# Kernel tuning notes

Hardware: AMD Instinct MI355X
Metric: run time of the kernel (lower is better)

Reference implementation:

```python
import jax, jax.numpy as jnp
import numpy as np

N_NODES = 100000
N_EDGES = 1600000
IN_DIM = 256
OUT_DIM = 128


def setup_inputs() -> dict:
    key = jax.random.key(0)
    k1, k2, k3, k4, k5 = jax.random.split(key, 5)
    h = jax.random.normal(k1, (N_NODES, IN_DIM), dtype=jnp.float32)
    # xavier_normal-ish scales for the two weight matrices
    W = jax.random.normal(k2, (IN_DIM, OUT_DIM), dtype=jnp.float32) * (2.0 / np.sqrt(IN_DIM + OUT_DIM))
    a = jax.random.normal(k3, (2 * OUT_DIM,), dtype=jnp.float32) * (2.0 / np.sqrt(2 * OUT_DIM + 1))
    src = jax.random.randint(k4, (N_EDGES,), 0, N_NODES, dtype=jnp.int32)
    dst = jax.random.randint(k5, (N_EDGES,), 0, N_NODES, dtype=jnp.int32)
    return {"h": h, "W": W, "a": a, "src": src, "dst": dst}


def reference(h, W, a, src, dst):
    n = h.shape[0]
    d = W.shape[1]
    z = h @ W  # [N, out_dim]
    # attn_fc([z_src || z_dst]) == z_src @ a[:d] + z_dst @ a[d:]
    el = z @ a[:d]  # [N]
    er = z @ a[d:]  # [N]
    e = jax.nn.leaky_relu(el[src] + er[dst])  # [E], torch default slope 0.01
    # per-destination (segment) softmax, numerically stable
    seg_max = jax.ops.segment_max(e, dst, num_segments=n)
    e_exp = jnp.exp(e - seg_max[dst])
    denom = jax.ops.segment_sum(e_exp, dst, num_segments=n)
    alpha = e_exp / denom[dst]  # [E]
    # weighted scatter-sum of source z into destinations
    h_out = jax.ops.segment_sum(alpha[:, None] * z[src], dst, num_segments=n)
    return h_out
```

## Files before the change

### kernel.cpp

```cpp
#include <hip/hip_runtime.h>
#include <cstdint>
#include <cstddef>

#define N_NODES 100000
#define N_EDGES 1600000
#define IN_DIM  256
#define OUT_DIM 128

#define NBUCK  196
#define BSHIFT 9
#define BNODES 512
#define BCAP   10240
#define EPB    4096

#define ENC_NEG_INF 0x00800000u
#define PAD_PAIR 0xFF7FFFFF00000000ull

typedef __attribute__((ext_vector_type(8))) short bf16x8;
typedef __attribute__((ext_vector_type(4))) float f32x4;

__device__ __forceinline__ unsigned bf16rn(float f) {
    unsigned u = __float_as_uint(f);
    return (u + 0x7FFFu + ((u >> 16) & 1u)) >> 16;
}

__global__ void init_k(int* __restrict__ bucket_cursor)
{
    int t = threadIdx.x;
    if (t < NBUCK) bucket_cursor[t] = 0;
}

__global__ void w16s_k(const float* __restrict__ W, unsigned short* __restrict__ w16s)
{
    int t = blockIdx.x * blockDim.x + threadIdx.x;
    if (t >= IN_DIM * OUT_DIM) return;
    int j  = t & 7;
    int n  = (t >> 3) & 15;
    int q  = (t >> 7) & 3;
    int c  = (t >> 9) & 7;
    int kc = t >> 12;
    int k   = kc * 32 + q * 8 + j;
    int dim = c * 16 + n;
    w16s[t] = (unsigned short)bf16rn(W[k * OUT_DIM + dim]);
}

#define LA_STRIDE 264

__global__ __launch_bounds__(256) void gemm_z_k(
    const float* __restrict__ h, const unsigned short* __restrict__ w16s,
    const float* __restrict__ a,
    unsigned short* __restrict__ z16, float* __restrict__ el, float* __restrict__ er)
{
    __shared__ unsigned short lA[64 * LA_STRIDE];
    const int t  = threadIdx.x;
    const int n0 = blockIdx.x * 64;

    #pragma unroll
    for (int p = 0; p < 16; ++p) {
        int f = p * 256 + t;
        int i = f >> 6;
        int col = (f & 63) * 4;
        float4 v = make_float4(0.f, 0.f, 0.f, 0.f);
        if (n0 + i < N_NODES)
            v = *(const float4*)&h[(size_t)(n0 + i) * IN_DIM + col];
        uint2 pk;
        pk.x = bf16rn(v.x) | (bf16rn(v.y) << 16);
        pk.y = bf16rn(v.z) | (bf16rn(v.w) << 16);
        *(uint2*)&lA[i * LA_STRIDE + col] = pk;
    }
    __syncthreads();

    const int w    = t >> 6;
    const int lane = t & 63;
    const int q    = lane >> 4;
    const int col  = lane & 15;

    f32x4 acc[8];
    #pragma unroll
    for (int c = 0; c < 8; ++c) acc[c] = (f32x4){0.f, 0.f, 0.f, 0.f};

    #pragma unroll
    for (int kc = 0; kc < 8; ++kc) {
        bf16x8 af = *(const bf16x8*)&lA[(w * 16 + col) * LA_STRIDE + kc * 32 + q * 8];
        bf16x8 bfr[8];
        #pragma unroll
        for (int c = 0; c < 8; ++c)
            bfr[c] = *(const bf16x8*)&w16s[((((kc * 8 + c) * 4 + q) * 16) + col) * 8];
        #pragma unroll
        for (int c = 0; c < 8; ++c)
            acc[c] = __builtin_amdgcn_mfma_f32_16x16x32_bf16(af, bfr[c], acc[c], 0, 0, 0);
    }

    float aL[8], aR[8];
    #pragma unroll
    for (int c = 0; c < 8; ++c) {
        aL[c] = a[c * 16 + col];
        aR[c] = a[128 + c * 16 + col];
    }
    #pragma unroll
    for (int r = 0; r < 4; ++r) {
        int node = n0 + w * 16 + q * 4 + r;
        float sl = 0.f, sr = 0.f;
        #pragma unroll
        for (int c = 0; c < 8; ++c) {
            sl += acc[c][r] * aL[c];
            sr += acc[c][r] * aR[c];
        }
        #pragma unroll
        for (int o = 1; o < 16; o <<= 1) {
            sl += __shfl_xor(sl, o, 64);
            sr += __shfl_xor(sr, o, 64);
        }
        if (node < N_NODES) {
            #pragma unroll
            for (int c = 0; c < 8; ++c)
                z16[(size_t)node * OUT_DIM + c * 16 + col] =
                    (unsigned short)bf16rn(acc[c][r]);
            if (col == 0) { el[node] = sl; er[node] = sr; }
        }
    }
}

__global__ __launch_bounds__(256) void partition_k(
    const int* __restrict__ src, const int* __restrict__ dst,
    const float* __restrict__ el, const float* __restrict__ er,
    int* __restrict__ bucket_cursor, unsigned long long* __restrict__ ebuf)
{
    __shared__ int hist[NBUCK];
    __shared__ int gbaseL[NBUCK];
    const int t = threadIdx.x;
    for (int i = t; i < NBUCK; i += 256) hist[i] = 0;
    __syncthreads();

    const int e0 = blockIdx.x * EPB;
    int bucks[16], ranks[16];
    unsigned long long pk[16];
    #pragma unroll
    for (int k = 0; k < 16; ++k) {
        int e = e0 + k * 256 + t;
        bucks[k] = -1;
        if (e < N_EDGES) {
            int s = src[e], d = dst[e];
            float v = el[s] + er[d];
            v = (v > 0.0f) ? v : 0.01f * v;
            int b = d >> BSHIFT;
            bucks[k] = b;
            ranks[k] = atomicAdd(&hist[b], 1);
            pk[k] = ((unsigned long long)__float_as_uint(v) << 32)
                  | ((unsigned)s << BSHIFT) | (unsigned)(d & (BNODES - 1));
        }
    }
    __syncthreads();
    for (int i = t; i < NBUCK; i += 256)
        gbaseL[i] = atomicAdd(&bucket_cursor[i], hist[i]);
    __syncthreads();
    #pragma unroll
    for (int k = 0; k < 16; ++k)
        if (bucks[k] >= 0)
            ebuf[(size_t)bucks[k] * BCAP + gbaseL[bucks[k]] + ranks[k]] = pk[k];
}

__global__ __launch_bounds__(256) void bucket_k(
    const int* __restrict__ bucket_cursor, const unsigned long long* __restrict__ ebuf,
    unsigned long long* __restrict__ perm, int* __restrict__ begA,
    int* __restrict__ endA, unsigned* __restrict__ emaxA)
{
    __shared__ int deg[BNODES];
    __shared__ int off[BNODES];
    __shared__ int cur[BNODES];
    __shared__ unsigned emaxL[BNODES];
    __shared__ int ssum[256];

    const int b = blockIdx.x;
    const int t = threadIdx.x;
    const int cnt = bucket_cursor[b];
    const unsigned long long* eb = ebuf + (size_t)b * BCAP;
    unsigned long long* pb = perm + (size_t)b * BCAP;

    for (int i = t; i < BNODES; i += 256) { deg[i] = 0; emaxL[i] = ENC_NEG_INF; }
    __syncthreads();

    for (int i = t; i < cnt; i += 256)
        atomicAdd(&deg[(int)(eb[i] & (BNODES - 1))], 1);
    __syncthreads();

    int d0 = deg[2 * t], d1 = deg[2 * t + 1];
    int p0 = (d0 + 3) & ~3, p1 = (d1 + 3) & ~3;
    ssum[t] = p0 + p1;
    __syncthreads();
    for (int o = 1; o < 256; o <<= 1) {
        int v = (t >= o) ? ssum[t - o] : 0;
        __syncthreads();
        ssum[t] += v;
        __syncthreads();
    }
    int excl = ssum[t] - (p0 + p1);
    off[2 * t] = excl;       cur[2 * t] = excl;
    off[2 * t + 1] = excl + p0; cur[2 * t + 1] = excl + p0;
    __syncthreads();

    for (int i = t; i < cnt; i += 256) {
        unsigned long long pv = eb[i];
        int ld = (int)(pv & (BNODES - 1));
        unsigned s  = (unsigned)((pv >> BSHIFT) & 0x1FFFFu);
        unsigned eb32 = (unsigned)(pv >> 32);
        int p = atomicAdd(&cur[ld], 1);
        pb[p] = ((unsigned long long)eb32 << 32) | s;
        unsigned enc = (eb32 & 0x80000000u) ? ~eb32 : (eb32 | 0x80000000u);
        atomicMax(&emaxL[ld], enc);
    }
    __syncthreads();

    for (int i = t; i < BNODES; i += 256) {
        int n = b * BNODES + i;
        if (n < N_NODES) {
            int d  = deg[i];
            int pd = (d + 3) & ~3;
            int o  = off[i];
            int gb = b * BCAP + o;
            begA[n]  = gb;
            endA[n]  = gb + pd;
            emaxA[n] = emaxL[i];
            for (int j = o + d; j < o + pd; ++j) pb[j] = PAD_PAIR;
        }
    }
}

__global__ __launch_bounds__(256) void node_pass_k(
    const int* __restrict__ begA, const int* __restrict__ endA,
    const unsigned* __restrict__ emaxA, const unsigned long long* __restrict__ perm,
    const unsigned* __restrict__ z16, float* __restrict__ out)
{
    int n    = (blockIdx.x * blockDim.x + threadIdx.x) >> 6;
    int lane = threadIdx.x & 63;
    if (n >= N_NODES) return;
    int beg = begA[n], end = endA[n];

    float acc0 = 0.0f, acc1 = 0.0f;
    if (end > beg) {
        unsigned u = emaxA[n];
        float mx = (u & 0x80000000u) ? __uint_as_float(u ^ 0x80000000u)
                                     : __uint_as_float(~u);
        float denom = 0.0f;
        const uint4* pp = (const uint4*)perm;
        #pragma unroll 2
        for (int i = (beg >> 2); i < (end >> 2); ++i) {
            uint4 pA = pp[2 * i];
            uint4 pB = pp[2 * i + 1];
            unsigned q0 = z16[(size_t)pA.x * 64 + lane];
            unsigned q1 = z16[(size_t)pA.z * 64 + lane];
            unsigned q2 = z16[(size_t)pB.x * 64 + lane];
            unsigned q3 = z16[(size_t)pB.z * 64 + lane];
            float w0 = __expf(__uint_as_float(pA.y) - mx);
            float w1 = __expf(__uint_as_float(pA.w) - mx);
            float w2 = __expf(__uint_as_float(pB.y) - mx);
            float w3 = __expf(__uint_as_float(pB.w) - mx);
            denom += (w0 + w1) + (w2 + w3);
            acc0 += w0 * __uint_as_float(q0 << 16)
                  + w1 * __uint_as_float(q1 << 16)
                  + w2 * __uint_as_float(q2 << 16)
                  + w3 * __uint_as_float(q3 << 16);
            acc1 += w0 * __uint_as_float(q0 & 0xFFFF0000u)
                  + w1 * __uint_as_float(q1 & 0xFFFF0000u)
                  + w2 * __uint_as_float(q2 & 0xFFFF0000u)
                  + w3 * __uint_as_float(q3 & 0xFFFF0000u);
        }
        float inv = 1.0f / denom;
        acc0 *= inv; acc1 *= inv;
    }
    *(float2*)&out[(size_t)n * OUT_DIM + lane * 2] = make_float2(acc0, acc1);
}

extern "C" void kernel_launch(void* const* d_in, const int* in_sizes, int n_in,
                              void* d_out, int out_size, void* d_ws, size_t ws_size,
                              hipStream_t stream)
{
    (void)in_sizes; (void)n_in; (void)out_size; (void)ws_size;
    const float* h = (const float*)d_in[0];
    const float* W = (const float*)d_in[1];
    const float* a = (const float*)d_in[2];
    const int* src = (const int*)d_in[3];
    const int* dst = (const int*)d_in[4];
    float* out = (float*)d_out;

    char* ws = (char*)d_ws;
    size_t off = 0;
    auto alloc = [&](size_t bytes) -> char* {
        char* p = ws + off;
        off += (bytes + 255) & ~(size_t)255;
        return p;
    };
    unsigned short* z16  = (unsigned short*)alloc((size_t)N_NODES * OUT_DIM * 2);
    unsigned short* w16s = (unsigned short*)alloc((size_t)IN_DIM * OUT_DIM * 2);
    float*    el        = (float*)   alloc((size_t)N_NODES * 4);
    float*    er        = (float*)   alloc((size_t)N_NODES * 4);
    int*      bucket_cursor = (int*) alloc((size_t)NBUCK * 4);
    unsigned long long* ebuf = (unsigned long long*)alloc((size_t)NBUCK * BCAP * 8);
    unsigned long long* perm = (unsigned long long*)alloc((size_t)NBUCK * BCAP * 8);
    int*      begA      = (int*)     alloc((size_t)N_NODES * 4);
    int*      endA      = (int*)     alloc((size_t)N_NODES * 4);
    unsigned* emaxA     = (unsigned*)alloc((size_t)N_NODES * 4);

    init_k<<<1, 256, 0, stream>>>(bucket_cursor);
    w16s_k<<<(IN_DIM * OUT_DIM + 255) / 256, 256, 0, stream>>>(W, w16s);
    gemm_z_k<<<(N_NODES + 63) / 64, 256, 0, stream>>>(h, w16s, a, z16, el, er);
    partition_k<<<(N_EDGES + EPB - 1) / EPB, 256, 0, stream>>>(src, dst, el, er,
                                                               bucket_cursor, ebuf);
    bucket_k<<<NBUCK, 256, 0, stream>>>(bucket_cursor, ebuf, perm, begA, endA, emaxA);
    node_pass_k<<<(N_NODES * 64 + 255) / 256, 256, 0, stream>>>(begA, endA, emaxA, perm,
                                                                (const unsigned*)z16, out);
}
```

Measured before the change: 309.8 us.

## Precompute softmax weights and denominators in bucket pass, halve bucket size

The bucket kernel now computes each destination's max in the counting pass, then evaluates exp(e - max) per edge, accumulates the per-node denominator in shared memory, and stores the weight instead of the raw score in the permuted edge array. The node pass then only does weighted gathers and one division, with no exp or denominator accumulation across the 64 lanes. Buckets shrink from 512 to 256 nodes, giving 391 blocks and one node per thread, which raises parallelism in the bucket kernel. The cost is an extra read of the bucket's edges, more shared-memory atomics, and a denominator summed by float atomics in nondeterministic order.

```diff
diff --git a/kernel.cpp b/kernel.cpp
--- a/kernel.cpp
+++ b/kernel.cpp
@@ -7,14 +7,13 @@
 #define IN_DIM  256
 #define OUT_DIM 128
 
-#define NBUCK  196
-#define BSHIFT 9
-#define BNODES 512
-#define BCAP   10240
+#define NBUCK  391
+#define BSHIFT 8
+#define BNODES 256
+#define BCAP   5632
 #define EPB    4096
 
 #define ENC_NEG_INF 0x00800000u
-#define PAD_PAIR 0xFF7FFFFF00000000ull
 
 typedef __attribute__((ext_vector_type(8))) short bf16x8;
 typedef __attribute__((ext_vector_type(4))) float f32x4;
@@ -26,8 +25,8 @@
 
 __global__ void init_k(int* __restrict__ bucket_cursor)
 {
-    int t = threadIdx.x;
-    if (t < NBUCK) bucket_cursor[t] = 0;
+    int i = blockIdx.x * blockDim.x + threadIdx.x;
+    if (i < NBUCK) bucket_cursor[i] = 0;
 }
 
 __global__ void w16s_k(const float* __restrict__ W, unsigned short* __restrict__ w16s)
@@ -163,12 +162,13 @@
 __global__ __launch_bounds__(256) void bucket_k(
     const int* __restrict__ bucket_cursor, const unsigned long long* __restrict__ ebuf,
     unsigned long long* __restrict__ perm, int* __restrict__ begA,
-    int* __restrict__ endA, unsigned* __restrict__ emaxA)
+    int* __restrict__ endA, float* __restrict__ denomA)
 {
     __shared__ int deg[BNODES];
     __shared__ int off[BNODES];
     __shared__ int cur[BNODES];
     __shared__ unsigned emaxL[BNODES];
+    __shared__ float denomL[BNODES];
     __shared__ int ssum[256];
 
     const int b = blockIdx.x;
@@ -177,16 +177,22 @@
     const unsigned long long* eb = ebuf + (size_t)b * BCAP;
     unsigned long long* pb = perm + (size_t)b * BCAP;
 
-    for (int i = t; i < BNODES; i += 256) { deg[i] = 0; emaxL[i] = ENC_NEG_INF; }
-    __syncthreads();
-
-    for (int i = t; i < cnt; i += 256)
-        atomicAdd(&deg[(int)(eb[i] & (BNODES - 1))], 1);
-    __syncthreads();
-
-    int d0 = deg[2 * t], d1 = deg[2 * t + 1];
-    int p0 = (d0 + 3) & ~3, p1 = (d1 + 3) & ~3;
-    ssum[t] = p0 + p1;
+    deg[t] = 0; emaxL[t] = ENC_NEG_INF; denomL[t] = 0.0f;
+    __syncthreads();
+
+    for (int i = t; i < cnt; i += 256) {
+        unsigned long long pv = eb[i];
+        int ld = (int)(pv & (BNODES - 1));
+        unsigned e32 = (unsigned)(pv >> 32);
+        unsigned enc = (e32 & 0x80000000u) ? ~e32 : (e32 | 0x80000000u);
+        atomicAdd(&deg[ld], 1);
+        atomicMax(&emaxL[ld], enc);
+    }
+    __syncthreads();
+
+    int d  = deg[t];
+    int pd = (d + 3) & ~3;
+    ssum[t] = pd;
     __syncthreads();
     for (int o = 1; o < 256; o <<= 1) {
         int v = (t >= o) ? ssum[t - o] : 0;
@@ -194,41 +200,39 @@
         ssum[t] += v;
         __syncthreads();
     }
-    int excl = ssum[t] - (p0 + p1);
-    off[2 * t] = excl;       cur[2 * t] = excl;
-    off[2 * t + 1] = excl + p0; cur[2 * t + 1] = excl + p0;
+    int excl = ssum[t] - pd;
+    off[t] = excl; cur[t] = excl;
     __syncthreads();
 
     for (int i = t; i < cnt; i += 256) {
         unsigned long long pv = eb[i];
         int ld = (int)(pv & (BNODES - 1));
-        unsigned s  = (unsigned)((pv >> BSHIFT) & 0x1FFFFu);
-        unsigned eb32 = (unsigned)(pv >> 32);
+        unsigned s = (unsigned)((pv >> BSHIFT) & 0x1FFFFu);
+        float e = __uint_as_float((unsigned)(pv >> 32));
+        unsigned u = emaxL[ld];
+        float mx = (u & 0x80000000u) ? __uint_as_float(u ^ 0x80000000u)
+                                     : __uint_as_float(~u);
+        float w = __expf(e - mx);
+        atomicAdd(&denomL[ld], w);
         int p = atomicAdd(&cur[ld], 1);
-        pb[p] = ((unsigned long long)eb32 << 32) | s;
-        unsigned enc = (eb32 & 0x80000000u) ? ~eb32 : (eb32 | 0x80000000u);
-        atomicMax(&emaxL[ld], enc);
-    }
-    __syncthreads();
-
-    for (int i = t; i < BNODES; i += 256) {
-        int n = b * BNODES + i;
-        if (n < N_NODES) {
-            int d  = deg[i];
-            int pd = (d + 3) & ~3;
-            int o  = off[i];
-            int gb = b * BCAP + o;
-            begA[n]  = gb;
-            endA[n]  = gb + pd;
-            emaxA[n] = emaxL[i];
-            for (int j = o + d; j < o + pd; ++j) pb[j] = PAD_PAIR;
-        }
+        pb[p] = ((unsigned long long)__float_as_uint(w) << 32) | s;
+    }
+    __syncthreads();
+
+    int n = b * BNODES + t;
+    if (n < N_NODES) {
+        int o  = off[t];
+        int gb = b * BCAP + o;
+        begA[n]   = gb;
+        endA[n]   = gb + pd;
+        denomA[n] = denomL[t];
+        for (int j = o + d; j < o + pd; ++j) pb[j] = 0ull;
     }
 }
 
 __global__ __launch_bounds__(256) void node_pass_k(
     const int* __restrict__ begA, const int* __restrict__ endA,
-    const unsigned* __restrict__ emaxA, const unsigned long long* __restrict__ perm,
+    const float* __restrict__ denomA, const unsigned long long* __restrict__ perm,
     const unsigned* __restrict__ z16, float* __restrict__ out)
 {
     int n    = (blockIdx.x * blockDim.x + threadIdx.x) >> 6;
@@ -238,10 +242,6 @@
 
     float acc0 = 0.0f, acc1 = 0.0f;
     if (end > beg) {
-        unsigned u = emaxA[n];
-        float mx = (u & 0x80000000u) ? __uint_as_float(u ^ 0x80000000u)
-                                     : __uint_as_float(~u);
-        float denom = 0.0f;
         const uint4* pp = (const uint4*)perm;
         #pragma unroll 2
         for (int i = (beg >> 2); i < (end >> 2); ++i) {
@@ -251,11 +251,10 @@
             unsigned q1 = z16[(size_t)pA.z * 64 + lane];
             unsigned q2 = z16[(size_t)pB.x * 64 + lane];
             unsigned q3 = z16[(size_t)pB.z * 64 + lane];
-            float w0 = __expf(__uint_as_float(pA.y) - mx);
-            float w1 = __expf(__uint_as_float(pA.w) - mx);
-            float w2 = __expf(__uint_as_float(pB.y) - mx);
-            float w3 = __expf(__uint_as_float(pB.w) - mx);
-            denom += (w0 + w1) + (w2 + w3);
+            float w0 = __uint_as_float(pA.y);
+            float w1 = __uint_as_float(pA.w);
+            float w2 = __uint_as_float(pB.y);
+            float w3 = __uint_as_float(pB.w);
             acc0 += w0 * __uint_as_float(q0 << 16)
                   + w1 * __uint_as_float(q1 << 16)
                   + w2 * __uint_as_float(q2 << 16)
@@ -265,7 +264,7 @@
                   + w2 * __uint_as_float(q2 & 0xFFFF0000u)
                   + w3 * __uint_as_float(q3 & 0xFFFF0000u);
         }
-        float inv = 1.0f / denom;
+        float inv = 1.0f / denomA[n];
         acc0 *= inv; acc1 *= inv;
     }
     *(float2*)&out[(size_t)n * OUT_DIM + lane * 2] = make_float2(acc0, acc1);
@@ -299,14 +298,14 @@
     unsigned long long* perm = (unsigned long long*)alloc((size_t)NBUCK * BCAP * 8);
     int*      begA      = (int*)     alloc((size_t)N_NODES * 4);
     int*      endA      = (int*)     alloc((size_t)N_NODES * 4);
-    unsigned* emaxA     = (unsigned*)alloc((size_t)N_NODES * 4);
-
-    init_k<<<1, 256, 0, stream>>>(bucket_cursor);
+    float*    denomA    = (float*)   alloc((size_t)N_NODES * 4);
+
+    init_k<<<(NBUCK + 255) / 256, 256, 0, stream>>>(bucket_cursor);
     w16s_k<<<(IN_DIM * OUT_DIM + 255) / 256, 256, 0, stream>>>(W, w16s);
     gemm_z_k<<<(N_NODES + 63) / 64, 256, 0, stream>>>(h, w16s, a, z16, el, er);
     partition_k<<<(N_EDGES + EPB - 1) / EPB, 256, 0, stream>>>(src, dst, el, er,
                                                                bucket_cursor, ebuf);
-    bucket_k<<<NBUCK, 256, 0, stream>>>(bucket_cursor, ebuf, perm, begA, endA, emaxA);
-    node_pass_k<<<(N_NODES * 64 + 255) / 256, 256, 0, stream>>>(begA, endA, emaxA, perm,
+    bucket_k<<<NBUCK, 256, 0, stream>>>(bucket_cursor, ebuf, perm, begA, endA, denomA);
+    node_pass_k<<<(N_NODES * 64 + 255) / 256, 256, 0, stream>>>(begA, endA, denomA, perm,
                                                                 (const unsigned*)z16, out);
 }
```

New measurement: 308.0 us. Within noise of the previous version (-0.6%).
